# Performance work log

Measured on AMD Instinct MI355X. Metric: run time of the kernel, lower is better.

## Reference

```python
import jax, jax.numpy as jnp
import numpy as np

K = 10  # neighbors (k = min(k, N-1); N=4096 >> 10)
EPS = 1e-5  # InstanceNorm eps (torch default)


def knn_idx(coords, k):
    # coords: [B,3,N] -> indices of k nearest neighbors (excluding self) [B,N,k]
    pts = coords.transpose(0, 2, 1)  # [B,N,3]
    sq = jnp.sum(pts * pts, axis=-1)  # [B,N]
    dist = sq[:, :, None] + sq[:, None, :] - 2.0 * jnp.einsum('bnc,bmc->bnm', pts, pts)
    dist = jnp.clip(dist, 1e-12)
    _, idx = jax.lax.top_k(-dist, k + 1)  # ascending distance, sorted
    return idx[:, :, 1:]  # drop self


def graph_feature(idx, feats):
    # feats: [B,C,N], idx: [B,N,k] -> [B,2C,N,k] = [center, neighbor-center]
    neigh = jax.vmap(lambda f, i: f[:, i])(feats, idx)  # [B,C,N,k]
    center = jnp.broadcast_to(feats[..., None], neigh.shape)
    return jnp.concatenate([center, neigh - center], axis=1)


def instance_norm(x):
    # x: [B,C,N,k]; normalize over spatial dims per (batch, channel), no affine
    mu = jnp.mean(x, axis=(2, 3), keepdims=True)
    var = jnp.var(x, axis=(2, 3), keepdims=True)
    return (x - mu) * jax.lax.rsqrt(var + EPS)


def lrelu(x):
    return jnp.where(x >= 0, x, 0.2 * x)


def setup_inputs() -> dict:
    key = jax.random.key(0)
    k1, k2, k3, k4, k5 = jax.random.split(key, 5)
    B, C, N = 4, 128, 4096
    coords = jax.random.normal(k1, (B, 3, N), dtype=jnp.float32)
    features = jax.random.normal(k2, (B, C, N), dtype=jnp.float32)
    W1 = jax.random.normal(k3, (C, 2 * C), dtype=jnp.float32) * 0.05
    W2 = jax.random.normal(k4, (2 * C, 2 * C), dtype=jnp.float32) * 0.05
    W3 = jax.random.normal(k5, (C, 4 * C), dtype=jnp.float32) * 0.05
    return {"coords": coords, "features": features, "W1": W1, "W2": W2, "W3": W3}


def reference(coords, features, W1, W2, W3):
    idx = knn_idx(coords, K)  # same KNN graph used by both EdgeConv stages
    x0 = features  # [B,C,N]
    # stage 1: EdgeConv C -> C
    g1 = graph_feature(idx, x0)  # [B,2C,N,k]
    x1 = lrelu(instance_norm(jnp.einsum('oc,bcnk->bonk', W1, g1)))
    x1 = jnp.max(x1, axis=-1)  # [B,C,N]
    # stage 2: EdgeConv C -> 2C
    g2 = graph_feature(idx, x1)  # [B,2C,N,k] (input C, cat -> 2C)
    x2 = lrelu(instance_norm(jnp.einsum('oc,bcnk->bonk', W2, g2)))
    x2 = jnp.max(x2, axis=-1)  # [B,2C,N]
    # fuse: [x0,x1,x2] -> 4C -> C via conv1x1 + InstanceNorm (spatial = N)
    x3 = jnp.concatenate([x0, x1, x2], axis=1)  # [B,4C,N]
    x3 = jnp.einsum('oc,bcn->bon', W3, x3)[..., None]  # [B,C,N,1]
    x3 = lrelu(instance_norm(x3))[..., 0]  # [B,C,N]
    return x3
```

## Files before the change

kernel.cpp:

```cpp
#include <hip/hip_runtime.h>
#include <math.h>
#include <stdint.h>

#define NB 4
#define NC 128
#define NP 4096
#define KNN 10


__device__ __forceinline__ uint16_t f2bf(float f) {
  uint32_t u = __float_as_uint(f);
  u += 0x7fffu + ((u >> 16) & 1u);
  return (uint16_t)(u >> 16);
}
__device__ __forceinline__ float bf2f(uint16_t h) {
  return __uint_as_float(((uint32_t)h) << 16);
}

__device__ __forceinline__ void async16(const void* g, void* l) {
  __builtin_amdgcn_global_load_lds(
      (const __attribute__((address_space(1))) unsigned int*)g,
      (__attribute__((address_space(3))) unsigned int*)l,
      16, 0, 0);
}

__device__ __forceinline__ uint32_t fsort(float f) {
  uint32_t u = __float_as_uint(f);
  return (u & 0x80000000u) ? ~u : (u | 0x80000000u);
}
__device__ __forceinline__ float funsort(uint32_t k) {
  uint32_t u = (k & 0x80000000u) ? (k & 0x7fffffffu) : ~k;
  return __uint_as_float(u);
}

typedef __bf16 bf16x8 __attribute__((ext_vector_type(8)));
typedef float f32x4 __attribute__((ext_vector_type(4)));

__global__ void k_prep(const float* __restrict__ W1, const float* __restrict__ W2,
                       const float* __restrict__ W3, const float* __restrict__ coords,
                       const float* __restrict__ feat,
                       uint16_t* __restrict__ Xcat,
                       uint16_t* __restrict__ W1cat, uint16_t* __restrict__ W2cat,
                       uint16_t* __restrict__ W3b,
                       float* __restrict__ stats, float4* __restrict__ pts4) {
  __shared__ float tile[32][33];
  int bid = blockIdx.x;
  if (bid < 2048) {
    int b = bid >> 9;
    int r = bid & 511;
    int n0 = (r >> 2) << 5;
    int c0 = (r & 3) << 5;
    int tx = threadIdx.x & 31, ty = threadIdx.x >> 5;
#pragma unroll
    for (int i = 0; i < 4; i++) {
      int c = c0 + ty + i * 8;
      tile[ty + i * 8][tx] = feat[(b * 128 + c) * 4096 + n0 + tx];
    }
    __syncthreads();
#pragma unroll
    for (int i = 0; i < 4; i++) {
      int n = n0 + ty + i * 8;
      Xcat[((b * 4096 + n) * 512) + c0 + tx] = f2bf(tile[tx][ty + i * 8]);
    }
    return;
  }
  int t = (bid - 2048) * 256 + threadIdx.x;
  if (t < 32768) {
    int o = t >> 7, c = t & 127;
    float v;
    if (o < 128) v = W1[o * 256 + c] - W1[o * 256 + 128 + c];
    else         v = W1[(o - 128) * 256 + 128 + c];
    W1cat[t] = f2bf(v);
  } else if (t < 98304) {
    int t2 = t - 32768;
    int o = t2 >> 7, c = t2 & 127;
    float v;
    if (o < 256) v = W2[o * 256 + c] - W2[o * 256 + 128 + c];
    else         v = W2[(o - 256) * 256 + 128 + c];
    W2cat[t2] = f2bf(v);
  } else if (t < 163840) {
    int t2 = t - 98304;
    W3b[t2] = f2bf(W3[t2]);
  } else if (t < 163840 + 8192) {
    stats[t - 163840] = 0.f;
  } else if (t < 163840 + 8192 + 16384) {
    int t2 = t - 163840 - 8192;
    int b = t2 >> 12, n = t2 & 4095;
    const float* cb = coords + b * 12288;
    float x = cb[n], y = cb[4096 + n], z = cb[8192 + n];
    float w = fmaf(x, x, fmaf(y, y, z * z));
    pts4[t2] = make_float4(x, y, z, w);
  }
}

__global__ void k_knn_thr(const float4* __restrict__ pts4, float* __restrict__ candd) {
  int L = blockIdx.x;
  int ch = L & 7;
  int qb = (L >> 3) & 15;
  int b = L >> 7;
  int m0 = ch << 7;
  const float4* pb = pts4 + b * 4096;
  int t = threadIdx.x;
  int q = (qb << 8) + t;
  float4 qp = pb[q];
  float d10[10];
#pragma unroll
  for (int i = 0; i < 10; i++) d10[i] = 1e30f;
#pragma unroll 2
  for (int mm = 0; mm < 128; mm++) {
    int m = m0 + mm;
    float4 p = pb[m];
    float dot = fmaf(qp.x, p.x, fmaf(qp.y, p.y, qp.z * p.z));
    float s = qp.w + p.w;
    float d = fmaf(-2.f, dot, s);
    d = (m == q) ? 1e30f : d;
    if (d < d10[9]) {
      float carry = d;
#pragma unroll
      for (int i = 0; i < 10; i++) {
        float lo = fminf(d10[i], carry);
        carry = fmaxf(d10[i], carry);
        d10[i] = lo;
      }
    }
  }
  int row = b * 4096 + q;
#pragma unroll
  for (int i = 0; i < 10; i++) candd[row * 80 + ch * 10 + i] = d10[i];
}

__global__ void k_knn_merge(const float* __restrict__ candd, float* __restrict__ tq) {
  int gw = blockIdx.x * 4 + (threadIdx.x >> 6);
  int l = threadIdx.x & 63;
  const float* cp = candd + (size_t)gw * 80;
  uint32_t k0 = fsort(cp[l]);
  uint32_t k1 = (l < 16) ? fsort(cp[64 + l]) : 0xFFFFFFFFu;
  uint32_t g = 0;
#pragma unroll
  for (int it = 0; it < 10; it++) {
    uint32_t m = k0 < k1 ? k0 : k1;
#pragma unroll
    for (int s = 1; s < 64; s <<= 1) {
      uint32_t o = __shfl_xor(m, s);
      m = o < m ? o : m;
    }
    g = m;
    if (it < 9) {
      if (k0 == m) k0 = 0xFFFFFFFFu;
      else if (k1 == m) k1 = 0xFFFFFFFFu;
    }
  }
  if (l == 0) tq[gw] = funsort(g);
}

#define CFCAP 112
#define DMARGIN 1e-3f
__global__ __launch_bounds__(512) void k_knn_cf(
    const float4* __restrict__ pts4, const float* __restrict__ tq,
    int* __restrict__ idxout) {
  __shared__ int candi[8 * CFCAP];
  __shared__ int ccnt[8];
  int blk = blockIdx.x;
  int b = blk >> 9;
  int qg = blk & 511;
  int t = threadIdx.x;
  if (t < 8) ccnt[t] = 0;
  const float4* pb = pts4 + b * 4096;
  int qbase = qg * 8;
  float q2x[8], q2y[8], q2z[8], rhs[8];
#pragma unroll
  for (int j = 0; j < 8; j++) {
    float4 qp = pb[qbase + j];
    q2x[j] = -2.f * qp.x; q2y[j] = -2.f * qp.y; q2z[j] = -2.f * qp.z;
    rhs[j] = tq[b * 4096 + qbase + j] + DMARGIN - qp.w;
  }
  __syncthreads();
#pragma unroll 4
  for (int c = 0; c < 8; c++) {
    float4 p = pb[c * 512 + t];
    int m = c * 512 + t;
#pragma unroll
    for (int j = 0; j < 8; j++) {
      float tt = fmaf(q2x[j], p.x, fmaf(q2y[j], p.y, fmaf(q2z[j], p.z, p.w)));
      if (tt <= rhs[j]) {
        int pos = atomicAdd(&ccnt[j], 1);
        if (pos < CFCAP) candi[j * CFCAP + pos] = m;
      }
    }
  }
  __syncthreads();
  int w = t >> 6;
  int l = t & 63;
  {
    int qloc = w;
    int q2 = qbase + qloc;
    float4 qp2 = pb[q2];
    int c = ccnt[qloc]; c = c < CFCAP ? c : CFCAP;
    unsigned long long k0 = ~0ULL, k1 = ~0ULL;
#pragma unroll
    for (int u = 0; u < 2; u++) {
      int j = u * 64 + l;
      if (j < c) {
        int m = candi[qloc * CFCAP + j];
        float4 p = pb[m];
        float dot = fmaf(qp2.x, p.x, fmaf(qp2.y, p.y, qp2.z * p.z));
        float s = qp2.w + p.w;
        float d = fmaf(-2.f, dot, s);
        d = (m == q2) ? 1e30f : d;
        unsigned long long key = (((unsigned long long)fsort(d)) << 32) | (uint32_t)m;
        if (u == 0) k0 = key; else k1 = key;
      }
    }
    uint32_t keep[10];
#pragma unroll
    for (int it = 0; it < 10; it++) {
      unsigned long long m = k0 < k1 ? k0 : k1;
#pragma unroll
      for (int s = 1; s < 64; s <<= 1) {
        unsigned long long o = __shfl_xor(m, s);
        m = o < m ? o : m;
      }
      keep[it] = (uint32_t)(m & 0xffffffffu);
      if (k0 == m) k0 = ~0ULL;
      else if (k1 == m) k1 = ~0ULL;
    }
    if (l == 0) {
      int orow = b * 4096 + q2;
#pragma unroll
      for (int i = 0; i < 10; i++) idxout[orow * 10 + i] = (int)keep[i];
    }
  }
}

__global__ __launch_bounds__(256) void k_gemm_bf(
    const uint16_t* __restrict__ Xb, int ldx, int xoff,
    const uint16_t* __restrict__ Wb, int ldw, int K,
    uint16_t* __restrict__ Ub, uint16_t* __restrict__ Vb,
    int voff, int uld, int vld) {
  __shared__ __align__(16) uint8_t lds[49152];
  const int t = threadIdx.x;
  const int l = t & 63;
  const int wid = t >> 6;
  const int wr = wid & 1, wc = wid >> 1;
  const int p0 = blockIdx.x * 128;
  const int o0 = blockIdx.y * 64;

  const int rA = l >> 3;
  const int cbp = ((l & 7) ^ rA) << 4;
  const int swl = (l & 7) << 4;

  f32x4 acc[4][2];
#pragma unroll
  for (int mi = 0; mi < 4; mi++)
#pragma unroll
    for (int ni = 0; ni < 2; ni++) acc[mi][ni] = (f32x4)0.f;

  auto stage = [&](int k0, int buf) {
    const uint16_t* Xs_ = Xb + (size_t)p0 * ldx + xoff + k0;
    const uint16_t* Ws_ = Wb + (size_t)o0 * ldw + k0;
#pragma unroll
    for (int cc = 0; cc < 4; cc++) {
      int c = wid * 4 + cc;
      const uint8_t* g = (const uint8_t*)(Xs_ + (size_t)(c * 8 + rA) * ldx) + cbp;
      async16(g, &lds[buf * 16384 + c * 1024]);
    }
#pragma unroll
    for (int cc = 0; cc < 2; cc++) {
      int c = wid * 2 + cc;
      const uint8_t* g = (const uint8_t*)(Ws_ + (size_t)(c * 8 + rA) * ldw) + cbp;
      async16(g, &lds[32768 + buf * 8192 + c * 1024]);
    }
  };

  auto compute = [&](int buf) {
    const uint8_t* Ab = &lds[buf * 16384];
    const uint8_t* Bb = &lds[32768 + buf * 8192];
#pragma unroll
    for (int ks = 0; ks < 2; ks++) {
      int cb = ks * 64 + ((l >> 4) << 4);
      bf16x8 bfr[2];
#pragma unroll
      for (int ni = 0; ni < 2; ni++) {
        int n = wc * 32 + ni * 16 + (l & 15);
        bfr[ni] = *(const bf16x8*)(Bb + n * 128 + (cb ^ swl));
      }
#pragma unroll
      for (int mi = 0; mi < 4; mi++) {
        int m = wr * 64 + mi * 16 + (l & 15);
        bf16x8 afr = *(const bf16x8*)(Ab + m * 128 + (cb ^ swl));
        acc[mi][0] = __builtin_amdgcn_mfma_f32_16x16x32_bf16(afr, bfr[0], acc[mi][0], 0, 0, 0);
        acc[mi][1] = __builtin_amdgcn_mfma_f32_16x16x32_bf16(afr, bfr[1], acc[mi][1], 0, 0, 0);
      }
    }
  };

  const int nsteps = K >> 6;
  stage(0, 0);
  for (int s = 0; s < nsteps; s++) {
    __syncthreads();
    if (s + 1 < nsteps) stage((s + 1) << 6, (s + 1) & 1);
    compute(s & 1);
  }

  const bool isv = (o0 >= voff);
#pragma unroll
  for (int mi = 0; mi < 4; mi++)
#pragma unroll
    for (int ni = 0; ni < 2; ni++) {
      int col = o0 + wc * 32 + ni * 16 + (l & 15);
      int row0 = p0 + wr * 64 + mi * 16 + (l >> 4) * 4;
#pragma unroll
      for (int j = 0; j < 4; j++) {
        if (isv) Vb[(size_t)(row0 + j) * vld + (col - voff)] = f2bf(acc[mi][ni][j]);
        else     Ub[(size_t)(row0 + j) * uld + col] = f2bf(acc[mi][ni][j]);
      }
    }
}

__global__ __launch_bounds__(256) void k_gemm3(
    const uint16_t* __restrict__ Xb, int ldx,
    const uint16_t* __restrict__ Wb, int ldw,
    float* __restrict__ Y, int ldy, int K,
    float* __restrict__ T1s, float* __restrict__ T2s) {
  __shared__ __align__(16) uint8_t lds[32768];
  const int t = threadIdx.x;
  const int l = t & 63;
  const int wid = t >> 6;
  const int p0 = blockIdx.x * 64;
  const int o0 = blockIdx.y * 64;

  const int rA = l >> 3;
  const int cbp = ((l & 7) ^ rA) << 4;
  const int swl = (l & 7) << 4;

  f32x4 acc[4];
#pragma unroll
  for (int mi = 0; mi < 4; mi++) acc[mi] = (f32x4)0.f;

  auto stage = [&](int k0, int buf) {
    const uint16_t* Xs_ = Xb + (size_t)p0 * ldx + k0;
    const uint16_t* Ws_ = Wb + (size_t)o0 * ldw + k0;
#pragma unroll
    for (int cc = 0; cc < 2; cc++) {
      int c = wid * 2 + cc;
      const uint8_t* g = (const uint8_t*)(Xs_ + (size_t)(c * 8 + rA) * ldx) + cbp;
      async16(g, &lds[buf * 16384 + c * 1024]);
    }
#pragma unroll
    for (int cc = 0; cc < 2; cc++) {
      int c = wid * 2 + cc;
      const uint8_t* g = (const uint8_t*)(Ws_ + (size_t)(c * 8 + rA) * ldw) + cbp;
      async16(g, &lds[buf * 16384 + 8192 + c * 1024]);
    }
  };

  auto compute = [&](int buf) {
    const uint8_t* Ab = &lds[buf * 16384];
    const uint8_t* Bb = &lds[buf * 16384 + 8192];
#pragma unroll
    for (int ks = 0; ks < 2; ks++) {
      int cb = ks * 64 + ((l >> 4) << 4);
      int n = wid * 16 + (l & 15);
      bf16x8 bfr = *(const bf16x8*)(Bb + n * 128 + (cb ^ swl));
#pragma unroll
      for (int mi = 0; mi < 4; mi++) {
        int m = mi * 16 + (l & 15);
        bf16x8 afr = *(const bf16x8*)(Ab + m * 128 + (cb ^ swl));
        acc[mi] = __builtin_amdgcn_mfma_f32_16x16x32_bf16(afr, bfr, acc[mi], 0, 0, 0);
      }
    }
  };

  const int nsteps = K >> 6;
  stage(0, 0);
  for (int s = 0; s < nsteps; s++) {
    __syncthreads();
    if (s + 1 < nsteps) stage((s + 1) << 6, (s + 1) & 1);
    compute(s & 1);
  }

  int col = o0 + wid * 16 + (l & 15);
#pragma unroll
  for (int mi = 0; mi < 4; mi++) {
    int row0 = p0 + mi * 16 + (l >> 4) * 4;
#pragma unroll
    for (int j = 0; j < 4; j++)
      Y[(size_t)(row0 + j) * ldy + col] = acc[mi][j];
  }
  int b = p0 >> 12;
  float a1 = 0.f, a2 = 0.f;
#pragma unroll
  for (int mi = 0; mi < 4; mi++)
#pragma unroll
    for (int j = 0; j < 4; j++) {
      float y = acc[mi][j];
      a1 += y;
      a2 = fmaf(y, y, a2);
    }
  a1 += __shfl_xor(a1, 16); a2 += __shfl_xor(a2, 16);
  a1 += __shfl_xor(a1, 32); a2 += __shfl_xor(a2, 32);
  if ((l >> 4) == 0) {
    atomicAdd(&T1s[b * 128 + col], a1);
    atomicAdd(&T2s[b * 128 + col], a2);
  }
}

template <int O>
__global__ void k_gather(const uint16_t* __restrict__ Ub,
                         const uint16_t* __restrict__ Vb,
                         const int* __restrict__ idx,
                         uint16_t* __restrict__ S,
                         float* __restrict__ T1, float* __restrict__ T2) {
  int L = blockIdx.x;
  int rx = L & 7;
  int b = rx >> 1;
  int j = ((L >> 3) << 1) + (rx & 1);
  int n0 = j << 4;
  int o = threadIdx.x;
  float a1 = 0.f, a2 = 0.f;
  for (int pi = 0; pi < 16; pi++) {
    int row = b * 4096 + n0 + pi;
    float u = bf2f(Ub[(size_t)row * O + o]);
    float s1 = 0.f, s2 = 0.f, vmax = -1e30f;
#pragma unroll
    for (int jj = 0; jj < KNN; jj++) {
      int m = idx[row * 10 + jj];
      float v = bf2f(Vb[(size_t)(b * 4096 + m) * O + o]);
      s1 += v;
      float x = u + v;
      s2 = fmaf(x, x, s2);
      vmax = fmaxf(vmax, v);
    }
    S[(size_t)row * O + o] = f2bf(u + vmax);
    a1 += 10.f * u + s1;
    a2 += s2;
  }
  atomicAdd(&T1[b * O + o], a1);
  atomicAdd(&T2[b * O + o], a2);
}

template <int O>
__global__ void k_passB(const uint16_t* __restrict__ S, int coff,
                        const float* __restrict__ T1, const float* __restrict__ T2,
                        uint16_t* __restrict__ Xcat) {
  int t = blockIdx.x * 256 + threadIdx.x;
  int o = t & (O - 1);
  int pn = t / O;
  int b = pn >> 12;
  float mu = T1[b * O + o] * (1.f / 40960.f);
  float e2 = T2[b * O + o] * (1.f / 40960.f);
  float inv = rsqrtf(e2 - mu * mu + 1e-5f);
  float x = (bf2f(S[(size_t)pn * O + o]) - mu) * inv;
  Xcat[pn * 512 + coff + o] = f2bf(x >= 0.f ? x : 0.2f * x);
}

__global__ void k_out(const float* __restrict__ Y3, const float* __restrict__ T1,
                      const float* __restrict__ T2, float* __restrict__ out) {
  __shared__ float tile[32][33];
  int bid = blockIdx.x;
  int b = bid >> 9;
  int r = bid & 511;
  int n0 = (r >> 2) << 5;
  int o0 = (r & 3) << 5;
  int tx = threadIdx.x & 31, ty = threadIdx.x >> 5;
  int o = o0 + tx;
  float mu = T1[b * 128 + o] * (1.f / 4096.f);
  float e2 = T2[b * 128 + o] * (1.f / 4096.f);
  float inv = rsqrtf(e2 - mu * mu + 1e-5f);
#pragma unroll
  for (int i = 0; i < 4; i++) {
    int n = n0 + ty + i * 8;
    float v = (Y3[(b * 4096 + n) * 128 + o] - mu) * inv;
    tile[ty + i * 8][tx] = v >= 0.f ? v : 0.2f * v;
  }
  __syncthreads();
#pragma unroll
  for (int i = 0; i < 4; i++) {
    int oo = o0 + ty + i * 8;
    out[(b * 128 + oo) * 4096 + n0 + tx] = tile[tx][ty + i * 8];
  }
}

extern "C" void kernel_launch(void* const* d_in, const int* in_sizes, int n_in,
                              void* d_out, int out_size, void* d_ws, size_t ws_size,
                              hipStream_t stream) {
  const float* coords   = (const float*)d_in[0];
  const float* features = (const float*)d_in[1];
  const float* W1       = (const float*)d_in[2];
  const float* W2       = (const float*)d_in[3];
  const float* W3       = (const float*)d_in[4];
  float* out = (float*)d_out;

  float*    ws    = (float*)d_ws;
  uint16_t* Xcat  = (uint16_t*)ws;
  float*    candd = ws + 4194304;
  float*    tq    = ws + 5505024;
  float4*   pts4  = (float4*)(ws + 5521408);
  uint16_t* Ub1   = (uint16_t*)(ws + 5586944);
  uint16_t* Ub2   = (uint16_t*)(ws + 6635520);
  uint16_t* Sbuf  = (uint16_t*)(ws + 12582912);
  float*    Y3    = ws + 14680064;
  int*      idxb  = (int*)(ws + 16777216);
  uint16_t* W1cat = (uint16_t*)(ws + 16941056);
  uint16_t* W2cat = (uint16_t*)(ws + 16957440);
  uint16_t* W3b   = (uint16_t*)(ws + 16990208);
  float*    stats = ws + 17022976;
  uint16_t* Vb1   = (uint16_t*)(ws + 17031168);
  uint16_t* Vb2   = (uint16_t*)(ws + 18079744);

  k_prep<<<2784, 256, 0, stream>>>(W1, W2, W3, coords, features, Xcat,
                                   W1cat, W2cat, W3b, stats, pts4);
  k_knn_thr<<<512, 256, 0, stream>>>(pts4, candd);
  k_knn_merge<<<4096, 256, 0, stream>>>(candd, tq);
  k_knn_cf<<<2048, 512, 0, stream>>>(pts4, tq, idxb);

  k_gemm_bf<<<dim3(128, 4), 256, 0, stream>>>(Xcat, 512, 0, W1cat, 128, 128,
                                              Ub1, Vb1, 128, 128, 128);
  k_gather<128><<<1024, 128, 0, stream>>>(Ub1, Vb1, idxb, Sbuf, stats + 0, stats + 512);
  k_passB<128><<<8192, 256, 0, stream>>>(Sbuf, 128, stats + 0, stats + 512, Xcat);

  k_gemm_bf<<<dim3(128, 8), 256, 0, stream>>>(Xcat, 512, 128, W2cat, 128, 128,
                                              Ub2, Vb2, 256, 256, 256);
  k_gather<256><<<1024, 256, 0, stream>>>(Ub2, Vb2, idxb, Sbuf, stats + 1024, stats + 2048);
  k_passB<256><<<16384, 256, 0, stream>>>(Sbuf, 256, stats + 1024, stats + 2048, Xcat);

  k_gemm3<<<dim3(256, 2), 256, 0, stream>>>(Xcat, 512, W3b, 512, Y3, 128, 512,
                                            stats + 3072, stats + 3584);
  k_out<<<2048, 256, 0, stream>>>(Y3, stats + 3072, stats + 3584, out);
}
```

Before: 158.4 us.

## Split KNN candidate filtering and top-k selection into separate kernels

The candidate-filter kernel now runs with 256 threads per block instead of 512 and writes per-query candidate lists and counts to global workspace. A new selection kernel then runs one wavefront per query to compute exact distances and pick the 10 nearest. Before, each block had 8 wavefronts doing selection for 8 queries, and the filter loop used 512 threads. The aim is to raise occupancy and decouple the two phases. The cost is an extra kernel launch plus a round trip of about 1.8M ints through global memory, and the new buffers reuse the Sbuf and Y3 regions.

```diff
diff --git a/kernel.cpp b/kernel.cpp
--- a/kernel.cpp
+++ b/kernel.cpp
@@ -155,9 +155,9 @@
 
 #define CFCAP 112
 #define DMARGIN 1e-3f
-__global__ __launch_bounds__(512) void k_knn_cf(
+__global__ __launch_bounds__(256) void k_knn_cf(
     const float4* __restrict__ pts4, const float* __restrict__ tq,
-    int* __restrict__ idxout) {
+    int* __restrict__ gcnt, int* __restrict__ gcandi) {
   __shared__ int candi[8 * CFCAP];
   __shared__ int ccnt[8];
   int blk = blockIdx.x;
@@ -176,9 +176,9 @@
   }
   __syncthreads();
 #pragma unroll 4
-  for (int c = 0; c < 8; c++) {
-    float4 p = pb[c * 512 + t];
-    int m = c * 512 + t;
+  for (int c = 0; c < 16; c++) {
+    float4 p = pb[c * 256 + t];
+    int m = c * 256 + t;
 #pragma unroll
     for (int j = 0; j < 8; j++) {
       float tt = fmaf(q2x[j], p.x, fmaf(q2y[j], p.y, fmaf(q2z[j], p.z, p.w)));
@@ -189,46 +189,55 @@
     }
   }
   __syncthreads();
-  int w = t >> 6;
-  int l = t & 63;
-  {
-    int qloc = w;
-    int q2 = qbase + qloc;
-    float4 qp2 = pb[q2];
-    int c = ccnt[qloc]; c = c < CFCAP ? c : CFCAP;
-    unsigned long long k0 = ~0ULL, k1 = ~0ULL;
-#pragma unroll
-    for (int u = 0; u < 2; u++) {
-      int j = u * 64 + l;
-      if (j < c) {
-        int m = candi[qloc * CFCAP + j];
-        float4 p = pb[m];
-        float dot = fmaf(qp2.x, p.x, fmaf(qp2.y, p.y, qp2.z * p.z));
-        float s = qp2.w + p.w;
-        float d = fmaf(-2.f, dot, s);
-        d = (m == q2) ? 1e30f : d;
-        unsigned long long key = (((unsigned long long)fsort(d)) << 32) | (uint32_t)m;
-        if (u == 0) k0 = key; else k1 = key;
-      }
-    }
-    uint32_t keep[10];
-#pragma unroll
-    for (int it = 0; it < 10; it++) {
-      unsigned long long m = k0 < k1 ? k0 : k1;
-#pragma unroll
-      for (int s = 1; s < 64; s <<= 1) {
-        unsigned long long o = __shfl_xor(m, s);
-        m = o < m ? o : m;
-      }
-      keep[it] = (uint32_t)(m & 0xffffffffu);
-      if (k0 == m) k0 = ~0ULL;
-      else if (k1 == m) k1 = ~0ULL;
-    }
-    if (l == 0) {
-      int orow = b * 4096 + q2;
-#pragma unroll
-      for (int i = 0; i < 10; i++) idxout[orow * 10 + i] = (int)keep[i];
-    }
+  int row0 = b * 4096 + qbase;
+  if (t < 8) gcnt[row0 + t] = ccnt[t];
+  for (int i = t; i < 8 * CFCAP; i += 256) {
+    int j = i / CFCAP, pos = i - j * CFCAP;
+    gcandi[(size_t)(row0 + j) * CFCAP + pos] = candi[i];
+  }
+}
+
+__global__ __launch_bounds__(256) void k_knn_sel(
+    const float4* __restrict__ pts4, const int* __restrict__ gcnt,
+    const int* __restrict__ gcandi, int* __restrict__ idxout) {
+  int gw = blockIdx.x * 4 + (threadIdx.x >> 6);
+  int l = threadIdx.x & 63;
+  int b = gw >> 12;
+  int q2 = gw & 4095;
+  const float4* pb = pts4 + b * 4096;
+  float4 qp2 = pb[q2];
+  int c = gcnt[gw]; c = c < CFCAP ? c : CFCAP;
+  unsigned long long k0 = ~0ULL, k1 = ~0ULL;
+#pragma unroll
+  for (int u = 0; u < 2; u++) {
+    int j = u * 64 + l;
+    if (j < c) {
+      int m = gcandi[(size_t)gw * CFCAP + j];
+      float4 p = pb[m];
+      float dot = fmaf(qp2.x, p.x, fmaf(qp2.y, p.y, qp2.z * p.z));
+      float s = qp2.w + p.w;
+      float d = fmaf(-2.f, dot, s);
+      d = (m == q2) ? 1e30f : d;
+      unsigned long long key = (((unsigned long long)fsort(d)) << 32) | (uint32_t)m;
+      if (u == 0) k0 = key; else k1 = key;
+    }
+  }
+  uint32_t keep[10];
+#pragma unroll
+  for (int it = 0; it < 10; it++) {
+    unsigned long long m = k0 < k1 ? k0 : k1;
+#pragma unroll
+    for (int s = 1; s < 64; s <<= 1) {
+      unsigned long long o = __shfl_xor(m, s);
+      m = o < m ? o : m;
+    }
+    keep[it] = (uint32_t)(m & 0xffffffffu);
+    if (k0 == m) k0 = ~0ULL;
+    else if (k1 == m) k1 = ~0ULL;
+  }
+  if (l == 0) {
+#pragma unroll
+    for (int i = 0; i < 10; i++) idxout[(size_t)gw * 10 + i] = (int)keep[i];
   }
 }
 
@@ -499,7 +508,9 @@
   uint16_t* Ub1   = (uint16_t*)(ws + 5586944);
   uint16_t* Ub2   = (uint16_t*)(ws + 6635520);
   uint16_t* Sbuf  = (uint16_t*)(ws + 12582912);
+  int*      gcandi= (int*)(ws + 12582912);
   float*    Y3    = ws + 14680064;
+  int*      gcnt  = (int*)(ws + 14680064);
   int*      idxb  = (int*)(ws + 16777216);
   uint16_t* W1cat = (uint16_t*)(ws + 16941056);
   uint16_t* W2cat = (uint16_t*)(ws + 16957440);
@@ -512,7 +523,8 @@
                                    W1cat, W2cat, W3b, stats, pts4);
   k_knn_thr<<<512, 256, 0, stream>>>(pts4, candd);
   k_knn_merge<<<4096, 256, 0, stream>>>(candd, tq);
-  k_knn_cf<<<2048, 512, 0, stream>>>(pts4, tq, idxb);
+  k_knn_cf<<<2048, 256, 0, stream>>>(pts4, tq, gcnt, gcandi);
+  k_knn_sel<<<4096, 256, 0, stream>>>(pts4, gcnt, gcandi, idxb);
 
   k_gemm_bf<<<dim3(128, 4), 256, 0, stream>>>(Xcat, 512, 0, W1cat, 128, 128,
                                               Ub1, Vb1, 128, 128, 128);
```

Result: slower. 169.2 us (+6.8%).
